# Kernel optimization log

Measured on AMD Instinct MI355X. Metric: run time of the kernel, lower is better.

The kernel has to match this reference:

```python
import jax, jax.numpy as jnp
import numpy as np
from jax import lax

FEAT = 384        # features
FFN = 768         # ffn_features (chunk=True -> halves of 384)
ZDIM = FFN // 2   # 384
HID = 192         # AE hidden
B, N = 4, 128
LN_EPS = 1e-5


def gelu(x):
    return jax.nn.gelu(x, approximate=False)  # torch nn.GELU default = exact erf


def setup_inputs() -> dict:
    key = jax.random.key(0)
    ks = jax.random.split(key, 12)

    def lin(k, fan_in, shape):
        bound = 1.0 / np.sqrt(fan_in)
        return jax.random.uniform(k, shape, jnp.float32, -bound, bound)

    return {
        "x": jax.random.normal(ks[0], (B, N, FEAT), jnp.float32),
        "U_w": lin(ks[1], FEAT, (FEAT, FFN)),
        "U_b": lin(ks[2], FEAT, (FFN,)),
        "ln_w": jnp.ones((ZDIM,), jnp.float32),
        "ln_b": jnp.zeros((ZDIM,), jnp.float32),
        "enc_w": lin(ks[3], ZDIM, (ZDIM, HID)),
        "enc_b": lin(ks[4], ZDIM, (HID,)),
        "dec_w": lin(ks[5], HID, (HID, ZDIM)),
        "dec_b": lin(ks[6], HID, (ZDIM,)),
        "V_w": lin(ks[7], ZDIM, (ZDIM, FEAT)),
        "V_b": lin(ks[8], ZDIM, (FEAT,)),
    }


def _ae(z, enc_w, enc_b, dec_w, dec_b):
    h = gelu(z @ enc_w + enc_b)
    return h @ dec_w + dec_b


def reference(x, U_w, U_b, ln_w, ln_b, enc_w, enc_b, dec_w, dec_b, V_w, V_b):
    h = gelu(x @ U_w + U_b)                    # (B,N,FFN)
    xh, z = jnp.split(h, 2, axis=-1)           # chunk=True: (B,N,ZDIM) each
    z = lax.stop_gradient(z)                   # z.detach()
    mu = jnp.mean(z, axis=-1, keepdims=True)
    var = jnp.var(z, axis=-1, keepdims=True)
    z = (z - mu) / jnp.sqrt(var + LN_EPS) * ln_w + ln_b

    n = z.shape[1]
    eye = jnp.eye(n, dtype=z.dtype)
    # z_mask[b,i,j,:] = z[b,j,:] if i==j else 0   (mask_type='zeros')
    z_mask = eye[None, :, :, None] * z[:, None, :, :]   # (B,N,N,ZDIM)
    preds = _ae(z_mask, enc_w, enc_b, dec_w, dec_b)      # (B,N,N,ZDIM)
    dist = jnp.einsum('bijf,bjf->bij', preds, z)         # (B,N,N)
    attn = lax.stop_gradient(jax.nn.softmax(dist, axis=-1))
    out = jnp.einsum('bij,bjf->bif', attn, xh)           # (B,N,ZDIM)
    return out @ V_w + V_b                               # (B,N,FEAT)
```

## Files before the change

### kernel.cpp

```cpp
#include <hip/hip_runtime.h>
#include <hip/hip_bf16.h>
#include <math.h>

#define FEAT 384
#define FFN  768
#define ZDIM 384
#define HID  192
#define BB   4
#define NN   128
#define BN   (BB*NN)

__device__ __forceinline__ float gelu_exact(float x) {
    return 0.5f * x * (1.0f + erff(x * 0.70710678118654752440f));
}

__device__ __forceinline__ float bflo(unsigned u) { return __uint_as_float(u << 16); }
__device__ __forceinline__ float bfhi(unsigned u) { return __uint_as_float(u & 0xFFFF0000u); }

template<bool F32>
__device__ __forceinline__ float ldg(const void* p, int i) {
    if constexpr (F32) return ((const float*)p)[i];
    return __uint_as_float(((unsigned)((const unsigned short*)p)[i]) << 16);
}
template<bool F32>
__device__ __forceinline__ void stg(void* p, size_t i, float v) {
    if constexpr (F32) ((float*)p)[i] = v;
    else ((__hip_bfloat16*)p)[i] = __float2bfloat16(v);
}

template<bool F32> struct V8;
template<> struct V8<true> {
    float4 a, b;
    __device__ __forceinline__ void load(const void* p, size_t off) {
        a = *(const float4*)((const float*)p + off);
        b = *(const float4*)((const float*)p + off + 4);
    }
    __device__ __forceinline__ float g(int i) const {
        return (i < 4) ? (&a.x)[i] : (&b.x)[i - 4];
    }
};
template<> struct V8<false> {
    uint4 u;
    __device__ __forceinline__ void load(const void* p, size_t off) {
        u = *(const uint4*)((const unsigned short*)p + off);
    }
    __device__ __forceinline__ float g(int i) const {
        const unsigned w = (&u.x)[i >> 1];
        return (i & 1) ? bfhi(w) : bflo(w);
    }
};
template<bool F32> struct V4;
template<> struct V4<true> {
    float4 a;
    __device__ __forceinline__ void load(const void* p, size_t off) {
        a = *(const float4*)((const float*)p + off);
    }
    __device__ __forceinline__ float g(int i) const { return (&a.x)[i]; }
};
template<> struct V4<false> {
    uint2 u;
    __device__ __forceinline__ void load(const void* p, size_t off) {
        u = *(const uint2*)((const unsigned short*)p + off);
    }
    __device__ __forceinline__ float g(int i) const {
        const unsigned w = (&u.x)[i >> 1];
        return (i & 1) ? bfhi(w) : bflo(w);
    }
};

__device__ __forceinline__ bool is_f32(const void* ln_w) {
    return ((const unsigned short*)ln_w)[0] == 0;
}

__device__ __forceinline__ float block_sum(float v, float* sm) {
    for (int o = 32; o > 0; o >>= 1) v += __shfl_down(v, o, 64);
    const int lane = threadIdx.x & 63, w = threadIdx.x >> 6;
    __syncthreads();
    if (lane == 0) sm[w] = v;
    __syncthreads();
    return sm[0] + sm[1] + sm[2] + sm[3] + sm[4] + sm[5];
}
__device__ __forceinline__ float2 block_sum2(float vx, float vy, float* sm) {
    for (int o = 32; o > 0; o >>= 1) {
        vx += __shfl_down(vx, o, 64);
        vy += __shfl_down(vy, o, 64);
    }
    const int lane = threadIdx.x & 63, w = threadIdx.x >> 6;
    __syncthreads();
    if (lane == 0) { sm[w] = vx; sm[w + 6] = vy; }
    __syncthreads();
    return make_float2(sm[0] + sm[1] + sm[2] + sm[3] + sm[4] + sm[5],
                       sm[6] + sm[7] + sm[8] + sm[9] + sm[10] + sm[11]);
}
__device__ __forceinline__ float block_max(float v, float* sm) {
    for (int o = 32; o > 0; o >>= 1) v = fmaxf(v, __shfl_down(v, o, 64));
    const int lane = threadIdx.x & 63, w = threadIdx.x >> 6;
    __syncthreads();
    if (lane == 0) sm[w] = v;
    __syncthreads();
    return fmaxf(fmaxf(fmaxf(sm[0], sm[1]), fmaxf(sm[2], sm[3])), fmaxf(sm[4], sm[5]));
}

template<bool F32>
__device__ void rows_body(
    const void* __restrict__ x, const void* __restrict__ U_w,
    const void* __restrict__ U_b, const void* __restrict__ ln_w,
    const void* __restrict__ ln_b, const void* __restrict__ enc_w,
    const void* __restrict__ enc_b, const void* __restrict__ dec_w,
    const void* __restrict__ dec_b, const void* __restrict__ V_w,
    float* __restrict__ Y, float* __restrict__ d0, float* __restrict__ diag)
{
    const int pr = blockIdx.x >> 1;
    const int h  = blockIdx.x & 1;
    const int r0 = 2 * pr, r1 = r0 + 1;
    const int t = threadIdx.x;
    __shared__ float xs[2][FEAT];
    __shared__ float zs[2][ZDIM];
    __shared__ float hid[2][HID];
    __shared__ float gh[HID];
    __shared__ float part[5376];
    __shared__ float sm[12];

    xs[0][t] = ldg<F32>(x, r0 * FEAT + t);
    xs[1][t] = ldg<F32>(x, r1 * FEAT + t);
    if (h && t < HID) gh[t] = gelu_exact(ldg<F32>(enc_b, t));
    __syncthreads();

    const int cg = t % 48, kh = t / 48;
    const int cL = 8 * cg;
    const int cG = 384 * h + cL;
    const int kb = 48 * kh;
    float a0[8] = {0,0,0,0,0,0,0,0}, a1[8] = {0,0,0,0,0,0,0,0};
    {
        V8<F32> wa[8], wb[8];
        #pragma unroll
        for (int j = 0; j < 8; j++) wa[j].load(U_w, (size_t)(kb + j) * FFN + cG);
        for (int k0 = kb; k0 < kb + 48; k0 += 16) {
            #pragma unroll
            for (int j = 0; j < 8; j++) wb[j].load(U_w, (size_t)(k0 + 8 + j) * FFN + cG);
            #pragma unroll
            for (int j = 0; j < 8; j++) {
                const float x0 = xs[0][k0 + j], x1 = xs[1][k0 + j];
                #pragma unroll
                for (int i = 0; i < 8; i++) {
                    const float w = wa[j].g(i);
                    a0[i] = fmaf(x0, w, a0[i]);
                    a1[i] = fmaf(x1, w, a1[i]);
                }
            }
            if (k0 + 16 < kb + 48) {
                #pragma unroll
                for (int j = 0; j < 8; j++) wa[j].load(U_w, (size_t)(k0 + 16 + j) * FFN + cG);
            }
            #pragma unroll
            for (int j = 0; j < 8; j++) {
                const float x0 = xs[0][k0 + 8 + j], x1 = xs[1][k0 + 8 + j];
                #pragma unroll
                for (int i = 0; i < 8; i++) {
                    const float w = wb[j].g(i);
                    a0[i] = fmaf(x0, w, a0[i]);
                    a1[i] = fmaf(x1, w, a1[i]);
                }
            }
        }
    }
    if (kh > 0) {
        float* p = &part[(kh - 1) * 768 + cg];
        #pragma unroll
        for (int i = 0; i < 8; i++) { p[i * 48] = a0[i]; p[384 + i * 48] = a1[i]; }
    }
    __syncthreads();

    float h0[8], h1[8];
    if (kh == 0) {
        #pragma unroll
        for (int i = 0; i < 8; i++) {
            const float ub = ldg<F32>(U_b, cG + i);
            float v0 = a0[i] + ub, v1 = a1[i] + ub;
            #pragma unroll
            for (int kk = 0; kk < 7; kk++) {
                v0 += part[kk * 768 + i * 48 + cg];
                v1 += part[kk * 768 + 384 + i * 48 + cg];
            }
            h0[i] = gelu_exact(v0);
            h1[i] = gelu_exact(v1);
        }
    }

    if (h == 0) {
        if (kh == 0) {
            #pragma unroll
            for (int i = 0; i < 8; i++) { zs[0][cL + i] = h0[i]; zs[1][cL + i] = h1[i]; }
        }
        __syncthreads();
        float y0[8] = {0,0,0,0,0,0,0,0}, y1[8] = {0,0,0,0,0,0,0,0};
        {
            V8<F32> va[8], vb[8];
            #pragma unroll
            for (int j = 0; j < 8; j++) va[j].load(V_w, (size_t)(kb + j) * FEAT + cL);
            for (int k0 = kb; k0 < kb + 48; k0 += 16) {
                #pragma unroll
                for (int j = 0; j < 8; j++) vb[j].load(V_w, (size_t)(k0 + 8 + j) * FEAT + cL);
                #pragma unroll
                for (int j = 0; j < 8; j++) {
                    const float s0 = zs[0][k0 + j], s1 = zs[1][k0 + j];
                    #pragma unroll
                    for (int i = 0; i < 8; i++) {
                        const float w = va[j].g(i);
                        y0[i] = fmaf(s0, w, y0[i]);
                        y1[i] = fmaf(s1, w, y1[i]);
                    }
                }
                if (k0 + 16 < kb + 48) {
                    #pragma unroll
                    for (int j = 0; j < 8; j++) va[j].load(V_w, (size_t)(k0 + 16 + j) * FEAT + cL);
                }
                #pragma unroll
                for (int j = 0; j < 8; j++) {
                    const float s0 = zs[0][k0 + 8 + j], s1 = zs[1][k0 + 8 + j];
                    #pragma unroll
                    for (int i = 0; i < 8; i++) {
                        const float w = vb[j].g(i);
                        y0[i] = fmaf(s0, w, y0[i]);
                        y1[i] = fmaf(s1, w, y1[i]);
                    }
                }
            }
        }
        if (kh > 0) {
            float* p = &part[(kh - 1) * 768 + cg];
            #pragma unroll
            for (int i = 0; i < 8; i++) { p[i * 48] = y0[i]; p[384 + i * 48] = y1[i]; }
        }
        __syncthreads();
        if (kh == 0) {
            float o0[8], o1[8];
            #pragma unroll
            for (int i = 0; i < 8; i++) {
                float u0 = y0[i], u1 = y1[i];
                #pragma unroll
                for (int kk = 0; kk < 7; kk++) {
                    u0 += part[kk * 768 + i * 48 + cg];
                    u1 += part[kk * 768 + 384 + i * 48 + cg];
                }
                o0[i] = u0; o1[i] = u1;
            }
            *(float4*)(Y + (size_t)r0 * FEAT + cL)     = make_float4(o0[0], o0[1], o0[2], o0[3]);
            *(float4*)(Y + (size_t)r0 * FEAT + cL + 4) = make_float4(o0[4], o0[5], o0[6], o0[7]);
            *(float4*)(Y + (size_t)r1 * FEAT + cL)     = make_float4(o1[0], o1[1], o1[2], o1[3]);
            *(float4*)(Y + (size_t)r1 * FEAT + cL + 4) = make_float4(o1[4], o1[5], o1[6], o1[7]);
        }
        return;
    }

    float s1a = 0.f, s1b = 0.f, s2a = 0.f, s2b = 0.f;
    if (kh == 0) {
        #pragma unroll
        for (int i = 0; i < 8; i++) {
            s1a += h0[i]; s2a += h0[i] * h0[i];
            s1b += h1[i]; s2b += h1[i] * h1[i];
        }
    }
    const float2 S1 = block_sum2(s1a, s1b, sm);
    const float2 S2 = block_sum2(s2a, s2b, sm);
    const float mu0 = S1.x * (1.0f / ZDIM), mu1 = S1.y * (1.0f / ZDIM);
    const float rs0 = rsqrtf(S2.x * (1.0f / ZDIM) - mu0 * mu0 + 1e-5f);
    const float rs1 = rsqrtf(S2.y * (1.0f / ZDIM) - mu1 * mu1 + 1e-5f);
    if (kh == 0) {
        #pragma unroll
        for (int i = 0; i < 8; i++) {
            const int zc = cL + i;
            const float w = ldg<F32>(ln_w, zc), bb = ldg<F32>(ln_b, zc);
            zs[0][zc] = (h0[i] - mu0) * rs0 * w + bb;
            zs[1][zc] = (h1[i] - mu1) * rs1 * w + bb;
        }
    }
    __syncthreads();

    {
        const int cgE = t % 48, khE = t / 48;
        const int cE = 4 * cgE, kbE = 48 * khE;
        float e0a[4] = {0,0,0,0}, e1a[4] = {0,0,0,0};
        V4<F32> va[8], vb[8];
        #pragma unroll
        for (int j = 0; j < 8; j++) va[j].load(enc_w, (size_t)(kbE + j) * HID + cE);
        for (int k0 = kbE; k0 < kbE + 48; k0 += 16) {
            #pragma unroll
            for (int j = 0; j < 8; j++) vb[j].load(enc_w, (size_t)(k0 + 8 + j) * HID + cE);
            #pragma unroll
            for (int j = 0; j < 8; j++) {
                const float z0 = zs[0][k0 + j], z1 = zs[1][k0 + j];
                #pragma unroll
                for (int i = 0; i < 4; i++) {
                    const float w = va[j].g(i);
                    e0a[i] = fmaf(z0, w, e0a[i]);
                    e1a[i] = fmaf(z1, w, e1a[i]);
                }
            }
            if (k0 + 16 < kbE + 48) {
                #pragma unroll
                for (int j = 0; j < 8; j++) va[j].load(enc_w, (size_t)(k0 + 16 + j) * HID + cE);
            }
            #pragma unroll
            for (int j = 0; j < 8; j++) {
                const float z0 = zs[0][k0 + 8 + j], z1 = zs[1][k0 + 8 + j];
                #pragma unroll
                for (int i = 0; i < 4; i++) {
                    const float w = vb[j].g(i);
                    e0a[i] = fmaf(z0, w, e0a[i]);
                    e1a[i] = fmaf(z1, w, e1a[i]);
                }
            }
        }
        if (khE > 0) {
            float* p = &part[(khE - 1) * 384 + cgE];
            #pragma unroll
            for (int i = 0; i < 4; i++) { p[i * 48] = e0a[i]; p[192 + i * 48] = e1a[i]; }
        }
        __syncthreads();
        if (khE == 0) {
            #pragma unroll
            for (int i = 0; i < 4; i++) {
                const float ebv = ldg<F32>(enc_b, cE + i);
                float v0 = e0a[i] + ebv, v1 = e1a[i] + ebv;
                #pragma unroll
                for (int kk = 0; kk < 7; kk++) {
                    v0 += part[kk * 384 + i * 48 + cgE];
                    v1 += part[kk * 384 + 192 + i * 48 + cgE];
                }
                hid[0][cE + i] = gelu_exact(v0);
                hid[1][cE + i] = gelu_exact(v1);
            }
        }
        __syncthreads();
    }

    {
        const int cgD = t % 96, khD = t / 96;
        const int cD = 4 * cgD, kbD = 48 * khD;
        float aa[4] = {0,0,0,0}, ab_[4] = {0,0,0,0}, ac[4] = {0,0,0,0};
        V4<F32> va[8], vb[8];
        #pragma unroll
        for (int j = 0; j < 8; j++) va[j].load(dec_w, (size_t)(kbD + j) * ZDIM + cD);
        for (int k0 = kbD; k0 < kbD + 48; k0 += 16) {
            #pragma unroll
            for (int j = 0; j < 8; j++) vb[j].load(dec_w, (size_t)(k0 + 8 + j) * ZDIM + cD);
            #pragma unroll
            for (int j = 0; j < 8; j++) {
                const float v0 = hid[0][k0 + j], v1 = hid[1][k0 + j], gv = gh[k0 + j];
                #pragma unroll
                for (int i = 0; i < 4; i++) {
                    const float w = va[j].g(i);
                    aa[i] = fmaf(v0, w, aa[i]);
                    ab_[i] = fmaf(v1, w, ab_[i]);
                    ac[i] = fmaf(gv, w, ac[i]);
                }
            }
            if (k0 + 16 < kbD + 48) {
                #pragma unroll
                for (int j = 0; j < 8; j++) va[j].load(dec_w, (size_t)(k0 + 16 + j) * ZDIM + cD);
            }
            #pragma unroll
            for (int j = 0; j < 8; j++) {
                const float v0 = hid[0][k0 + 8 + j], v1 = hid[1][k0 + 8 + j], gv = gh[k0 + 8 + j];
                #pragma unroll
                for (int i = 0; i < 4; i++) {
                    const float w = vb[j].g(i);
                    aa[i] = fmaf(v0, w, aa[i]);
                    ab_[i] = fmaf(v1, w, ab_[i]);
                    ac[i] = fmaf(gv, w, ac[i]);
                }
            }
        }
        if (khD > 0) {
            float* p = &part[(khD - 1) * 1152 + cgD];
            #pragma unroll
            for (int i = 0; i < 4; i++) {
                p[i * 96] = aa[i];
                p[384 + i * 96] = ab_[i];
                p[768 + i * 96] = ac[i];
            }
        }
        __syncthreads();
        float pd0 = 0.f, pd1 = 0.f, pe0 = 0.f, pe1 = 0.f;
        if (khD == 0) {
            #pragma unroll
            for (int i = 0; i < 4; i++) {
                const int c = cD + i;
                const float dbv = ldg<F32>(dec_b, c);
                float v0 = aa[i] + dbv, v1 = ab_[i] + dbv, v2 = ac[i] + dbv;
                #pragma unroll
                for (int kk = 0; kk < 3; kk++) {
                    v0 += part[kk * 1152 + i * 96 + cgD];
                    v1 += part[kk * 1152 + 384 + i * 96 + cgD];
                    v2 += part[kk * 1152 + 768 + i * 96 + cgD];
                }
                const float z0 = zs[0][c], z1 = zs[1][c];
                pd0 = fmaf(v0, z0, pd0);
                pd1 = fmaf(v1, z1, pd1);
                pe0 = fmaf(v2, z0, pe0);
                pe1 = fmaf(v2, z1, pe1);
            }
        }
        const float2 DG = block_sum2(pd0, pd1, sm);
        const float2 DD = block_sum2(pe0, pe1, sm);
        if (t == 0) {
            diag[r0] = DG.x; diag[r1] = DG.y;
            d0[r0] = DD.x;   d0[r1] = DD.y;
        }
    }
}

__global__ __launch_bounds__(384) void k_rows(
    const void* x, const void* U_w, const void* U_b,
    const void* ln_w, const void* ln_b,
    const void* enc_w, const void* enc_b,
    const void* dec_w, const void* dec_b, const void* V_w,
    float* Y, float* d0, float* diag)
{
    if (is_f32(ln_w))
        rows_body<true >(x, U_w, U_b, ln_w, ln_b, enc_w, enc_b, dec_w, dec_b, V_w, Y, d0, diag);
    else
        rows_body<false>(x, U_w, U_b, ln_w, ln_b, enc_w, enc_b, dec_w, dec_b, V_w, Y, d0, diag);
}

template<bool F32>
__device__ void combine_body(
    const float* __restrict__ d0, const float* __restrict__ diag,
    const float* __restrict__ Y,
    const void* __restrict__ V_b, void* __restrict__ out)
{
    const int b  = blockIdx.x >> 2;
    const int cc = (blockIdx.x & 3) * 96;
    const int t = threadIdx.x;
    const int c = t % 96, q = t / 96;
    __shared__ float e0s[NN], eds[NN];
    __shared__ float bp[4 * 96];
    __shared__ float baseY[96];
    __shared__ float sm[12];

    float d0v = -INFINITY, dgv = -INFINITY;
    if (t < NN) { d0v = d0[b * NN + t]; dgv = diag[b * NN + t]; }
    const float m = block_max(fmaxf(d0v, dgv), sm);
    float e0v = 0.f;
    if (t < NN) {
        e0v = expf(d0v - m);
        e0s[t] = e0v;
        eds[t] = expf(dgv - m);
    }
    const float S = block_sum(e0v, sm);

    const float* Yb = Y + (size_t)b * NN * FEAT + cc + c;
    const int j0 = 32 * q;
    float p = 0.f;
    for (int jj = 0; jj < 32; jj += 8) {
        float w[8];
        #pragma unroll
        for (int j = 0; j < 8; j++) w[j] = Yb[(size_t)(j0 + jj + j) * FEAT];
        #pragma unroll
        for (int j = 0; j < 8; j++) p = fmaf(e0s[j0 + jj + j], w[j], p);
    }
    bp[q * 96 + c] = p;
    __syncthreads();
    if (q == 0) baseY[c] = bp[c] + bp[96 + c] + bp[192 + c] + bp[288 + c];
    __syncthreads();

    const float bY = baseY[c];
    const float vb = ldg<F32>(V_b, cc + c);
    for (int rr = 0; rr < 32; rr += 8) {
        float w[8];
        #pragma unroll
        for (int j = 0; j < 8; j++) w[j] = Yb[(size_t)(j0 + rr + j) * FEAT];
        #pragma unroll
        for (int j = 0; j < 8; j++) {
            const int r = j0 + rr + j;
            const float inv = 1.0f / (S - e0s[r] + eds[r]);
            const float val = (bY + (eds[r] - e0s[r]) * w[j]) * inv + vb;
            stg<F32>(out, (size_t)(b * NN + r) * FEAT + cc + c, val);
        }
    }
}

__global__ __launch_bounds__(384) void k_combine(
    const void* ln_w,
    const float* d0, const float* diag, const float* Y,
    const void* V_b, void* out)
{
    if (is_f32(ln_w))
        combine_body<true >(d0, diag, Y, V_b, out);
    else
        combine_body<false>(d0, diag, Y, V_b, out);
}

extern "C" void kernel_launch(void* const* d_in, const int* in_sizes, int n_in,
                              void* d_out, int out_size, void* d_ws, size_t ws_size,
                              hipStream_t stream) {
    const void* x     = d_in[0];
    const void* U_w   = d_in[1];
    const void* U_b   = d_in[2];
    const void* ln_w  = d_in[3];
    const void* ln_b  = d_in[4];
    const void* enc_w = d_in[5];
    const void* enc_b = d_in[6];
    const void* dec_w = d_in[7];
    const void* dec_b = d_in[8];
    const void* V_w   = d_in[9];
    const void* V_b   = d_in[10];

    float* ws   = (float*)d_ws;
    float* Y    = ws;
    float* d0   = Y + (size_t)BN * FEAT;
    float* diag = d0 + BN;

    k_rows<<<BN, 384, 0, stream>>>(x, U_w, U_b, ln_w, ln_b, enc_w, enc_b,
                                   dec_w, dec_b, V_w, Y, d0, diag);
    k_combine<<<4 * BB, 384, 0, stream>>>(ln_w, d0, diag, Y, V_b, d_out);
}
```

Before: 117.6 us.

## Process four rows per block with 4x4 register-tiled GEMM helper

```diff
diff --git a/kernel.cpp b/kernel.cpp
--- a/kernel.cpp
+++ b/kernel.cpp
@@ -28,27 +28,6 @@
     else ((__hip_bfloat16*)p)[i] = __float2bfloat16(v);
 }
 
-template<bool F32> struct V8;
-template<> struct V8<true> {
-    float4 a, b;
-    __device__ __forceinline__ void load(const void* p, size_t off) {
-        a = *(const float4*)((const float*)p + off);
-        b = *(const float4*)((const float*)p + off + 4);
-    }
-    __device__ __forceinline__ float g(int i) const {
-        return (i < 4) ? (&a.x)[i] : (&b.x)[i - 4];
-    }
-};
-template<> struct V8<false> {
-    uint4 u;
-    __device__ __forceinline__ void load(const void* p, size_t off) {
-        u = *(const uint4*)((const unsigned short*)p + off);
-    }
-    __device__ __forceinline__ float g(int i) const {
-        const unsigned w = (&u.x)[i >> 1];
-        return (i & 1) ? bfhi(w) : bflo(w);
-    }
-};
 template<bool F32> struct V4;
 template<> struct V4<true> {
     float4 a;
@@ -80,18 +59,6 @@
     __syncthreads();
     return sm[0] + sm[1] + sm[2] + sm[3] + sm[4] + sm[5];
 }
-__device__ __forceinline__ float2 block_sum2(float vx, float vy, float* sm) {
-    for (int o = 32; o > 0; o >>= 1) {
-        vx += __shfl_down(vx, o, 64);
-        vy += __shfl_down(vy, o, 64);
-    }
-    const int lane = threadIdx.x & 63, w = threadIdx.x >> 6;
-    __syncthreads();
-    if (lane == 0) { sm[w] = vx; sm[w + 6] = vy; }
-    __syncthreads();
-    return make_float2(sm[0] + sm[1] + sm[2] + sm[3] + sm[4] + sm[5],
-                       sm[6] + sm[7] + sm[8] + sm[9] + sm[10] + sm[11]);
-}
 __device__ __forceinline__ float block_max(float v, float* sm) {
     for (int o = 32; o > 0; o >>= 1) v = fmaxf(v, __shfl_down(v, o, 64));
     const int lane = threadIdx.x & 63, w = threadIdx.x >> 6;
@@ -100,179 +67,128 @@
     __syncthreads();
     return fmaxf(fmaxf(fmaxf(sm[0], sm[1]), fmaxf(sm[2], sm[3])), fmaxf(sm[4], sm[5]));
 }
+__device__ __forceinline__ void block_sum4(float v0, float v1, float v2, float v3,
+                                           float* sm, float out[4]) {
+    for (int o = 32; o > 0; o >>= 1) {
+        v0 += __shfl_down(v0, o, 64);
+        v1 += __shfl_down(v1, o, 64);
+        v2 += __shfl_down(v2, o, 64);
+        v3 += __shfl_down(v3, o, 64);
+    }
+    const int lane = threadIdx.x & 63, w = threadIdx.x >> 6;
+    __syncthreads();
+    if (lane == 0) { sm[w] = v0; sm[6 + w] = v1; sm[12 + w] = v2; sm[18 + w] = v3; }
+    __syncthreads();
+    #pragma unroll
+    for (int q = 0; q < 4; q++)
+        out[q] = sm[q*6] + sm[q*6+1] + sm[q*6+2] + sm[q*6+3] + sm[q*6+4] + sm[q*6+5];
+}
+
+#define SM_TOTAL 9816
+
+template<bool F32, int KCH>
+__device__ __forceinline__ void gemm4x4(
+    const void* __restrict__ W, int ldw, int c0, int kb,
+    const float* __restrict__ in, int ldin, float acc[4][4])
+{
+    V4<F32> wa[8], wb[8];
+    #pragma unroll
+    for (int j = 0; j < 8; j++) wa[j].load(W, (size_t)(kb + j) * ldw + c0);
+    for (int k0 = kb; k0 < kb + KCH; k0 += 16) {
+        #pragma unroll
+        for (int j = 0; j < 8; j++) wb[j].load(W, (size_t)(k0 + 8 + j) * ldw + c0);
+        #pragma unroll
+        for (int j = 0; j < 8; j++) {
+            #pragma unroll
+            for (int m = 0; m < 4; m++) {
+                const float xv = in[m * ldin + k0 + j];
+                #pragma unroll
+                for (int i = 0; i < 4; i++) acc[m][i] = fmaf(xv, wa[j].g(i), acc[m][i]);
+            }
+        }
+        if (k0 + 16 < kb + KCH) {
+            #pragma unroll
+            for (int j = 0; j < 8; j++) wa[j].load(W, (size_t)(k0 + 16 + j) * ldw + c0);
+        }
+        #pragma unroll
+        for (int j = 0; j < 8; j++) {
+            #pragma unroll
+            for (int m = 0; m < 4; m++) {
+                const float xv = in[m * ldin + k0 + 8 + j];
+                #pragma unroll
+                for (int i = 0; i < 4; i++) acc[m][i] = fmaf(xv, wb[j].g(i), acc[m][i]);
+            }
+        }
+    }
+}
 
 template<bool F32>
-__device__ void rows_body(
+__device__ void bodyA(float* S, int q,
     const void* __restrict__ x, const void* __restrict__ U_w,
     const void* __restrict__ U_b, const void* __restrict__ ln_w,
     const void* __restrict__ ln_b, const void* __restrict__ enc_w,
     const void* __restrict__ enc_b, const void* __restrict__ dec_w,
-    const void* __restrict__ dec_b, const void* __restrict__ V_w,
-    float* __restrict__ Y, float* __restrict__ d0, float* __restrict__ diag)
-{
-    const int pr = blockIdx.x >> 1;
-    const int h  = blockIdx.x & 1;
-    const int r0 = 2 * pr, r1 = r0 + 1;
+    const void* __restrict__ dec_b,
+    float* __restrict__ d0, float* __restrict__ diag)
+{
+    const int rb = 4 * q;
     const int t = threadIdx.x;
-    __shared__ float xs[2][FEAT];
-    __shared__ float zs[2][ZDIM];
-    __shared__ float hid[2][HID];
-    __shared__ float gh[HID];
-    __shared__ float part[5376];
-    __shared__ float sm[12];
-
-    xs[0][t] = ldg<F32>(x, r0 * FEAT + t);
-    xs[1][t] = ldg<F32>(x, r1 * FEAT + t);
-    if (h && t < HID) gh[t] = gelu_exact(ldg<F32>(enc_b, t));
-    __syncthreads();
-
-    const int cg = t % 48, kh = t / 48;
-    const int cL = 8 * cg;
-    const int cG = 384 * h + cL;
-    const int kb = 48 * kh;
-    float a0[8] = {0,0,0,0,0,0,0,0}, a1[8] = {0,0,0,0,0,0,0,0};
-    {
-        V8<F32> wa[8], wb[8];
-        #pragma unroll
-        for (int j = 0; j < 8; j++) wa[j].load(U_w, (size_t)(kb + j) * FFN + cG);
-        for (int k0 = kb; k0 < kb + 48; k0 += 16) {
-            #pragma unroll
-            for (int j = 0; j < 8; j++) wb[j].load(U_w, (size_t)(k0 + 8 + j) * FFN + cG);
-            #pragma unroll
-            for (int j = 0; j < 8; j++) {
-                const float x0 = xs[0][k0 + j], x1 = xs[1][k0 + j];
-                #pragma unroll
-                for (int i = 0; i < 8; i++) {
-                    const float w = wa[j].g(i);
-                    a0[i] = fmaf(x0, w, a0[i]);
-                    a1[i] = fmaf(x1, w, a1[i]);
-                }
-            }
-            if (k0 + 16 < kb + 48) {
-                #pragma unroll
-                for (int j = 0; j < 8; j++) wa[j].load(U_w, (size_t)(k0 + 16 + j) * FFN + cG);
-            }
-            #pragma unroll
-            for (int j = 0; j < 8; j++) {
-                const float x0 = xs[0][k0 + 8 + j], x1 = xs[1][k0 + 8 + j];
-                #pragma unroll
-                for (int i = 0; i < 8; i++) {
-                    const float w = wb[j].g(i);
-                    a0[i] = fmaf(x0, w, a0[i]);
-                    a1[i] = fmaf(x1, w, a1[i]);
-                }
-            }
-        }
-    }
+    float* xs = S;
+    float* zs = S + 1536;
+    float* hid = S + 3072;
+    float* gh = S + 3840;
+    float* part = S + 4032;
+    float* sm = S + 9792;
+
+    #pragma unroll
+    for (int m = 0; m < 4; m++) xs[m * 384 + t] = ldg<F32>(x, (rb + m) * FEAT + t);
+    if (t < HID) gh[t] = gelu_exact(ldg<F32>(enc_b, t));
+    __syncthreads();
+
+    const int cg = t % 96, kh = t / 96;
+    const int cL = 4 * cg, cG = ZDIM + cL, kb = 96 * kh;
+    float acc[4][4] = {};
+    gemm4x4<F32, 96>(U_w, FFN, cG, kb, xs, 384, acc);
     if (kh > 0) {
-        float* p = &part[(kh - 1) * 768 + cg];
-        #pragma unroll
-        for (int i = 0; i < 8; i++) { p[i * 48] = a0[i]; p[384 + i * 48] = a1[i]; }
-    }
-    __syncthreads();
-
-    float h0[8], h1[8];
+        float* p = &part[(kh - 1) * 1536 + cg];
+        #pragma unroll
+        for (int m = 0; m < 4; m++)
+            #pragma unroll
+            for (int i = 0; i < 4; i++) p[(m * 4 + i) * 96] = acc[m][i];
+    }
+    __syncthreads();
+
+    float hv[4][4];
+    float s1[4] = {0,0,0,0}, s2[4] = {0,0,0,0};
     if (kh == 0) {
         #pragma unroll
-        for (int i = 0; i < 8; i++) {
+        for (int i = 0; i < 4; i++) {
             const float ub = ldg<F32>(U_b, cG + i);
-            float v0 = a0[i] + ub, v1 = a1[i] + ub;
-            #pragma unroll
-            for (int kk = 0; kk < 7; kk++) {
-                v0 += part[kk * 768 + i * 48 + cg];
-                v1 += part[kk * 768 + 384 + i * 48 + cg];
-            }
-            h0[i] = gelu_exact(v0);
-            h1[i] = gelu_exact(v1);
-        }
-    }
-
-    if (h == 0) {
-        if (kh == 0) {
-            #pragma unroll
-            for (int i = 0; i < 8; i++) { zs[0][cL + i] = h0[i]; zs[1][cL + i] = h1[i]; }
-        }
-        __syncthreads();
-        float y0[8] = {0,0,0,0,0,0,0,0}, y1[8] = {0,0,0,0,0,0,0,0};
-        {
-            V8<F32> va[8], vb[8];
-            #pragma unroll
-            for (int j = 0; j < 8; j++) va[j].load(V_w, (size_t)(kb + j) * FEAT + cL);
-            for (int k0 = kb; k0 < kb + 48; k0 += 16) {
-                #pragma unroll
-                for (int j = 0; j < 8; j++) vb[j].load(V_w, (size_t)(k0 + 8 + j) * FEAT + cL);
-                #pragma unroll
-                for (int j = 0; j < 8; j++) {
-                    const float s0 = zs[0][k0 + j], s1 = zs[1][k0 + j];
-                    #pragma unroll
-                    for (int i = 0; i < 8; i++) {
-                        const float w = va[j].g(i);
-                        y0[i] = fmaf(s0, w, y0[i]);
-                        y1[i] = fmaf(s1, w, y1[i]);
-                    }
-                }
-                if (k0 + 16 < kb + 48) {
-                    #pragma unroll
-                    for (int j = 0; j < 8; j++) va[j].load(V_w, (size_t)(k0 + 16 + j) * FEAT + cL);
-                }
-                #pragma unroll
-                for (int j = 0; j < 8; j++) {
-                    const float s0 = zs[0][k0 + 8 + j], s1 = zs[1][k0 + 8 + j];
-                    #pragma unroll
-                    for (int i = 0; i < 8; i++) {
-                        const float w = vb[j].g(i);
-                        y0[i] = fmaf(s0, w, y0[i]);
-                        y1[i] = fmaf(s1, w, y1[i]);
-                    }
-                }
-            }
-        }
-        if (kh > 0) {
-            float* p = &part[(kh - 1) * 768 + cg];
-            #pragma unroll
-            for (int i = 0; i < 8; i++) { p[i * 48] = y0[i]; p[384 + i * 48] = y1[i]; }
-        }
-        __syncthreads();
-        if (kh == 0) {
-            float o0[8], o1[8];
-            #pragma unroll
-            for (int i = 0; i < 8; i++) {
-                float u0 = y0[i], u1 = y1[i];
-                #pragma unroll
-                for (int kk = 0; kk < 7; kk++) {
-                    u0 += part[kk * 768 + i * 48 + cg];
-                    u1 += part[kk * 768 + 384 + i * 48 + cg];
-                }
-                o0[i] = u0; o1[i] = u1;
-            }
-            *(float4*)(Y + (size_t)r0 * FEAT + cL)     = make_float4(o0[0], o0[1], o0[2], o0[3]);
-            *(float4*)(Y + (size_t)r0 * FEAT + cL + 4) = make_float4(o0[4], o0[5], o0[6], o0[7]);
-            *(float4*)(Y + (size_t)r1 * FEAT + cL)     = make_float4(o1[0], o1[1], o1[2], o1[3]);
-            *(float4*)(Y + (size_t)r1 * FEAT + cL + 4) = make_float4(o1[4], o1[5], o1[6], o1[7]);
-        }
-        return;
-    }
-
-    float s1a = 0.f, s1b = 0.f, s2a = 0.f, s2b = 0.f;
+            #pragma unroll
+            for (int m = 0; m < 4; m++) {
+                float v = acc[m][i] + ub
+                        + part[(m * 4 + i) * 96 + cg]
+                        + part[1536 + (m * 4 + i) * 96 + cg]
+                        + part[3072 + (m * 4 + i) * 96 + cg];
+                v = gelu_exact(v);
+                hv[m][i] = v;
+                s1[m] += v; s2[m] += v * v;
+            }
+        }
+    }
+    float S1[4], S2[4];
+    block_sum4(s1[0], s1[1], s1[2], s1[3], sm, S1);
+    block_sum4(s2[0], s2[1], s2[2], s2[3], sm, S2);
     if (kh == 0) {
         #pragma unroll
-        for (int i = 0; i < 8; i++) {
-            s1a += h0[i]; s2a += h0[i] * h0[i];
-            s1b += h1[i]; s2b += h1[i] * h1[i];
-        }
-    }
-    const float2 S1 = block_sum2(s1a, s1b, sm);
-    const float2 S2 = block_sum2(s2a, s2b, sm);
-    const float mu0 = S1.x * (1.0f / ZDIM), mu1 = S1.y * (1.0f / ZDIM);
-    const float rs0 = rsqrtf(S2.x * (1.0f / ZDIM) - mu0 * mu0 + 1e-5f);
-    const float rs1 = rsqrtf(S2.y * (1.0f / ZDIM) - mu1 * mu1 + 1e-5f);
-    if (kh == 0) {
-        #pragma unroll
-        for (int i = 0; i < 8; i++) {
-            const int zc = cL + i;
-            const float w = ldg<F32>(ln_w, zc), bb = ldg<F32>(ln_b, zc);
-            zs[0][zc] = (h0[i] - mu0) * rs0 * w + bb;
-            zs[1][zc] = (h1[i] - mu1) * rs1 * w + bb;
+        for (int m = 0; m < 4; m++) {
+            const float mu = S1[m] * (1.0f / ZDIM);
+            const float rs = rsqrtf(S2[m] * (1.0f / ZDIM) - mu * mu + 1e-5f);
+            #pragma unroll
+            for (int i = 0; i < 4; i++) {
+                const int zc = cL + i;
+                zs[m * 384 + zc] = (hv[m][i] - mu) * rs * ldg<F32>(ln_w, zc) + ldg<F32>(ln_b, zc);
+            }
         }
     }
     __syncthreads();
@@ -280,56 +196,28 @@
     {
         const int cgE = t % 48, khE = t / 48;
         const int cE = 4 * cgE, kbE = 48 * khE;
-        float e0a[4] = {0,0,0,0}, e1a[4] = {0,0,0,0};
-        V4<F32> va[8], vb[8];
-        #pragma unroll
-        for (int j = 0; j < 8; j++) va[j].load(enc_w, (size_t)(kbE + j) * HID + cE);
-        for (int k0 = kbE; k0 < kbE + 48; k0 += 16) {
-            #pragma unroll
-            for (int j = 0; j < 8; j++) vb[j].load(enc_w, (size_t)(k0 + 8 + j) * HID + cE);
-            #pragma unroll
-            for (int j = 0; j < 8; j++) {
-                const float z0 = zs[0][k0 + j], z1 = zs[1][k0 + j];
-                #pragma unroll
-                for (int i = 0; i < 4; i++) {
-                    const float w = va[j].g(i);
-                    e0a[i] = fmaf(z0, w, e0a[i]);
-                    e1a[i] = fmaf(z1, w, e1a[i]);
-                }
-            }
-            if (k0 + 16 < kbE + 48) {
-                #pragma unroll
-                for (int j = 0; j < 8; j++) va[j].load(enc_w, (size_t)(k0 + 16 + j) * HID + cE);
-            }
-            #pragma unroll
-            for (int j = 0; j < 8; j++) {
-                const float z0 = zs[0][k0 + 8 + j], z1 = zs[1][k0 + 8 + j];
-                #pragma unroll
-                for (int i = 0; i < 4; i++) {
-                    const float w = vb[j].g(i);
-                    e0a[i] = fmaf(z0, w, e0a[i]);
-                    e1a[i] = fmaf(z1, w, e1a[i]);
-                }
-            }
-        }
+        float ea[4][4] = {};
+        gemm4x4<F32, 48>(enc_w, HID, cE, kbE, zs, 384, ea);
         if (khE > 0) {
-            float* p = &part[(khE - 1) * 384 + cgE];
-            #pragma unroll
-            for (int i = 0; i < 4; i++) { p[i * 48] = e0a[i]; p[192 + i * 48] = e1a[i]; }
+            float* p = &part[(khE - 1) * 768 + cgE];
+            #pragma unroll
+            for (int m = 0; m < 4; m++)
+                #pragma unroll
+                for (int i = 0; i < 4; i++) p[(m * 4 + i) * 48] = ea[m][i];
         }
         __syncthreads();
         if (khE == 0) {
             #pragma unroll
             for (int i = 0; i < 4; i++) {
                 const float ebv = ldg<F32>(enc_b, cE + i);
-                float v0 = e0a[i] + ebv, v1 = e1a[i] + ebv;
-                #pragma unroll
-                for (int kk = 0; kk < 7; kk++) {
-                    v0 += part[kk * 384 + i * 48 + cgE];
-                    v1 += part[kk * 384 + 192 + i * 48 + cgE];
+                #pragma unroll
+                for (int m = 0; m < 4; m++) {
+                    float v = ea[m][i] + ebv;
+                    #pragma unroll
+                    for (int kk = 0; kk < 7; kk++)
+                        v += part[kk * 768 + (m * 4 + i) * 48 + cgE];
+                    hid[m * 192 + cE + i] = gelu_exact(v);
                 }
-                hid[0][cE + i] = gelu_exact(v0);
-                hid[1][cE + i] = gelu_exact(v1);
             }
         }
         __syncthreads();
@@ -338,90 +226,174 @@
     {
         const int cgD = t % 96, khD = t / 96;
         const int cD = 4 * cgD, kbD = 48 * khD;
-        float aa[4] = {0,0,0,0}, ab_[4] = {0,0,0,0}, ac[4] = {0,0,0,0};
-        V4<F32> va[8], vb[8];
-        #pragma unroll
-        for (int j = 0; j < 8; j++) va[j].load(dec_w, (size_t)(kbD + j) * ZDIM + cD);
-        for (int k0 = kbD; k0 < kbD + 48; k0 += 16) {
-            #pragma unroll
-            for (int j = 0; j < 8; j++) vb[j].load(dec_w, (size_t)(k0 + 8 + j) * ZDIM + cD);
-            #pragma unroll
-            for (int j = 0; j < 8; j++) {
-                const float v0 = hid[0][k0 + j], v1 = hid[1][k0 + j], gv = gh[k0 + j];
-                #pragma unroll
-                for (int i = 0; i < 4; i++) {
-                    const float w = va[j].g(i);
-                    aa[i] = fmaf(v0, w, aa[i]);
-                    ab_[i] = fmaf(v1, w, ab_[i]);
-                    ac[i] = fmaf(gv, w, ac[i]);
+        float da[4][4] = {};
+        float dc[4] = {0,0,0,0};
+        {
+            V4<F32> wa[8], wb[8];
+            #pragma unroll
+            for (int j = 0; j < 8; j++) wa[j].load(dec_w, (size_t)(kbD + j) * ZDIM + cD);
+            for (int k0 = kbD; k0 < kbD + 48; k0 += 16) {
+                #pragma unroll
+                for (int j = 0; j < 8; j++) wb[j].load(dec_w, (size_t)(k0 + 8 + j) * ZDIM + cD);
+                #pragma unroll
+                for (int j = 0; j < 8; j++) {
+                    const float gv = gh[k0 + j];
+                    #pragma unroll
+                    for (int i = 0; i < 4; i++) {
+                        const float w = wa[j].g(i);
+                        dc[i] = fmaf(gv, w, dc[i]);
+                        #pragma unroll
+                        for (int m = 0; m < 4; m++)
+                            da[m][i] = fmaf(hid[m * 192 + k0 + j], w, da[m][i]);
+                    }
                 }
-            }
-            if (k0 + 16 < kbD + 48) {
-                #pragma unroll
-                for (int j = 0; j < 8; j++) va[j].load(dec_w, (size_t)(k0 + 16 + j) * ZDIM + cD);
-            }
-            #pragma unroll
-            for (int j = 0; j < 8; j++) {
-                const float v0 = hid[0][k0 + 8 + j], v1 = hid[1][k0 + 8 + j], gv = gh[k0 + 8 + j];
-                #pragma unroll
-                for (int i = 0; i < 4; i++) {
-                    const float w = vb[j].g(i);
-                    aa[i] = fmaf(v0, w, aa[i]);
-                    ab_[i] = fmaf(v1, w, ab_[i]);
-                    ac[i] = fmaf(gv, w, ac[i]);
+                if (k0 + 16 < kbD + 48) {
+                    #pragma unroll
+                    for (int j = 0; j < 8; j++) wa[j].load(dec_w, (size_t)(k0 + 16 + j) * ZDIM + cD);
                 }
+                #pragma unroll
+                for (int j = 0; j < 8; j++) {
+                    const float gv = gh[k0 + 8 + j];
+                    #pragma unroll
+                    for (int i = 0; i < 4; i++) {
+                        const float w = wb[j].g(i);
+                        dc[i] = fmaf(gv, w, dc[i]);
+                        #pragma unroll
+                        for (int m = 0; m < 4; m++)
+                            da[m][i] = fmaf(hid[m * 192 + k0 + 8 + j], w, da[m][i]);
+                    }
+                }
             }
         }
         if (khD > 0) {
-            float* p = &part[(khD - 1) * 1152 + cgD];
-            #pragma unroll
-            for (int i = 0; i < 4; i++) {
-                p[i * 96] = aa[i];
-                p[384 + i * 96] = ab_[i];
-                p[768 + i * 96] = ac[i];
-            }
+            float* p = &part[(khD - 1) * 1920 + cgD];
+            #pragma unroll
+            for (int m = 0; m < 4; m++)
+                #pragma unroll
+                for (int i = 0; i < 4; i++) p[(m * 4 + i) * 96] = da[m][i];
+            #pragma unroll
+            for (int i = 0; i < 4; i++) p[(16 + i) * 96] = dc[i];
         }
         __syncthreads();
-        float pd0 = 0.f, pd1 = 0.f, pe0 = 0.f, pe1 = 0.f;
+        float pd[4] = {0,0,0,0}, pe[4] = {0,0,0,0};
         if (khD == 0) {
             #pragma unroll
             for (int i = 0; i < 4; i++) {
                 const int c = cD + i;
                 const float dbv = ldg<F32>(dec_b, c);
-                float v0 = aa[i] + dbv, v1 = ab_[i] + dbv, v2 = ac[i] + dbv;
-                #pragma unroll
-                for (int kk = 0; kk < 3; kk++) {
-                    v0 += part[kk * 1152 + i * 96 + cgD];
-                    v1 += part[kk * 1152 + 384 + i * 96 + cgD];
-                    v2 += part[kk * 1152 + 768 + i * 96 + cgD];
+                float vc = dc[i] + dbv;
+                #pragma unroll
+                for (int kk = 0; kk < 3; kk++)
+                    vc += part[kk * 1920 + (16 + i) * 96 + cgD];
+                #pragma unroll
+                for (int m = 0; m < 4; m++) {
+                    float v = da[m][i] + dbv;
+                    #pragma unroll
+                    for (int kk = 0; kk < 3; kk++)
+                        v += part[kk * 1920 + (m * 4 + i) * 96 + cgD];
+                    const float zv = zs[m * 384 + c];
+                    pd[m] = fmaf(v, zv, pd[m]);
+                    pe[m] = fmaf(vc, zv, pe[m]);
                 }
-                const float z0 = zs[0][c], z1 = zs[1][c];
-                pd0 = fmaf(v0, z0, pd0);
-                pd1 = fmaf(v1, z1, pd1);
-                pe0 = fmaf(v2, z0, pe0);
-                pe1 = fmaf(v2, z1, pe1);
-            }
-        }
-        const float2 DG = block_sum2(pd0, pd1, sm);
-        const float2 DD = block_sum2(pe0, pe1, sm);
+            }
+        }
+        float DG[4], DD[4];
+        block_sum4(pd[0], pd[1], pd[2], pd[3], sm, DG);
+        block_sum4(pe[0], pe[1], pe[2], pe[3], sm, DD);
         if (t == 0) {
-            diag[r0] = DG.x; diag[r1] = DG.y;
-            d0[r0] = DD.x;   d0[r1] = DD.y;
-        }
-    }
-}
-
-__global__ __launch_bounds__(384) void k_rows(
+            #pragma unroll
+            for (int m = 0; m < 4; m++) { diag[rb + m] = DG[m]; d0[rb + m] = DD[m]; }
+        }
+    }
+}
+
+template<bool F32>
+__device__ void bodyB(float* S, int q,
+    const void* __restrict__ x, const void* __restrict__ U_w,
+    const void* __restrict__ U_b, const void* __restrict__ V_w,
+    float* __restrict__ Y)
+{
+    const int rb = 4 * q;
+    const int t = threadIdx.x;
+    float* xs = S;
+    float* zs = S + 1536;
+    float* part = S + 4032;
+
+    #pragma unroll
+    for (int m = 0; m < 4; m++) xs[m * 384 + t] = ldg<F32>(x, (rb + m) * FEAT + t);
+    __syncthreads();
+
+    const int cg = t % 96, kh = t / 96;
+    const int cL = 4 * cg, kb = 96 * kh;
+    float acc[4][4] = {};
+    gemm4x4<F32, 96>(U_w, FFN, cL, kb, xs, 384, acc);
+    if (kh > 0) {
+        float* p = &part[(kh - 1) * 1536 + cg];
+        #pragma unroll
+        for (int m = 0; m < 4; m++)
+            #pragma unroll
+            for (int i = 0; i < 4; i++) p[(m * 4 + i) * 96] = acc[m][i];
+    }
+    __syncthreads();
+    if (kh == 0) {
+        #pragma unroll
+        for (int i = 0; i < 4; i++) {
+            const float ub = ldg<F32>(U_b, cL + i);
+            #pragma unroll
+            for (int m = 0; m < 4; m++) {
+                float v = acc[m][i] + ub
+                        + part[(m * 4 + i) * 96 + cg]
+                        + part[1536 + (m * 4 + i) * 96 + cg]
+                        + part[3072 + (m * 4 + i) * 96 + cg];
+                zs[m * 384 + cL + i] = gelu_exact(v);
+            }
+        }
+    }
+    __syncthreads();
+
+    float ya[4][4] = {};
+    gemm4x4<F32, 96>(V_w, FEAT, cL, kb, zs, 384, ya);
+    if (kh > 0) {
+        float* p = &part[(kh - 1) * 1536 + cg];
+        #pragma unroll
+        for (int m = 0; m < 4; m++)
+            #pragma unroll
+            for (int i = 0; i < 4; i++) p[(m * 4 + i) * 96] = ya[m][i];
+    }
+    __syncthreads();
+    if (kh == 0) {
+        #pragma unroll
+        for (int m = 0; m < 4; m++) {
+            float o[4];
+            #pragma unroll
+            for (int i = 0; i < 4; i++) {
+                o[i] = ya[m][i]
+                     + part[(m * 4 + i) * 96 + cg]
+                     + part[1536 + (m * 4 + i) * 96 + cg]
+                     + part[3072 + (m * 4 + i) * 96 + cg];
+            }
+            *(float4*)(Y + (size_t)(rb + m) * FEAT + cL) = make_float4(o[0], o[1], o[2], o[3]);
+        }
+    }
+}
+
+__global__ __launch_bounds__(384) void k_main(
     const void* x, const void* U_w, const void* U_b,
     const void* ln_w, const void* ln_b,
     const void* enc_w, const void* enc_b,
     const void* dec_w, const void* dec_b, const void* V_w,
     float* Y, float* d0, float* diag)
 {
-    if (is_f32(ln_w))
-        rows_body<true >(x, U_w, U_b, ln_w, ln_b, enc_w, enc_b, dec_w, dec_b, V_w, Y, d0, diag);
-    else
-        rows_body<false>(x, U_w, U_b, ln_w, ln_b, enc_w, enc_b, dec_w, dec_b, V_w, Y, d0, diag);
+    __shared__ float S[SM_TOTAL];
+    const int type = blockIdx.x & 1;
+    const int q = blockIdx.x >> 1;
+    if (is_f32(ln_w)) {
+        if (type == 0) bodyA<true >(S, q, x, U_w, U_b, ln_w, ln_b, enc_w, enc_b, dec_w, dec_b, d0, diag);
+        else           bodyB<true >(S, q, x, U_w, U_b, V_w, Y);
+    } else {
+        if (type == 0) bodyA<false>(S, q, x, U_w, U_b, ln_w, ln_b, enc_w, enc_b, dec_w, dec_b, d0, diag);
+        else           bodyB<false>(S, q, x, U_w, U_b, V_w, Y);
+    }
 }
 
 template<bool F32>
@@ -433,7 +405,7 @@
     const int b  = blockIdx.x >> 2;
     const int cc = (blockIdx.x & 3) * 96;
     const int t = threadIdx.x;
-    const int c = t % 96, q = t / 96;
+    const int c = t % 96, qq = t / 96;
     __shared__ float e0s[NN], eds[NN];
     __shared__ float bp[4 * 96];
     __shared__ float baseY[96];
@@ -451,7 +423,7 @@
     const float S = block_sum(e0v, sm);
 
     const float* Yb = Y + (size_t)b * NN * FEAT + cc + c;
-    const int j0 = 32 * q;
+    const int j0 = 32 * qq;
     float p = 0.f;
     for (int jj = 0; jj < 32; jj += 8) {
         float w[8];
@@ -460,9 +432,9 @@
         #pragma unroll
         for (int j = 0; j < 8; j++) p = fmaf(e0s[j0 + jj + j], w[j], p);
     }
-    bp[q * 96 + c] = p;
-    __syncthreads();
-    if (q == 0) baseY[c] = bp[c] + bp[96 + c] + bp[192 + c] + bp[288 + c];
+    bp[qq * 96 + c] = p;
+    __syncthreads();
+    if (qq == 0) baseY[c] = bp[c] + bp[96 + c] + bp[192 + c] + bp[288 + c];
     __syncthreads();
 
     const float bY = baseY[c];
@@ -512,7 +484,7 @@
     float* d0   = Y + (size_t)BN * FEAT;
     float* diag = d0 + BN;
 
-    k_rows<<<BN, 384, 0, stream>>>(x, U_w, U_b, ln_w, ln_b, enc_w, enc_b,
-                                   dec_w, dec_b, V_w, Y, d0, diag);
+    k_main<<<2 * (BN / 4), 384, 0, stream>>>(x, U_w, U_b, ln_w, ln_b, enc_w, enc_b,
+                                             dec_w, dec_b, V_w, Y, d0, diag);
     k_combine<<<4 * BB, 384, 0, stream>>>(ln_w, d0, diag, Y, V_b, d_out);
 }
```

New measurement: 103.8 us. -11.7%, faster.
